# Performance work log

Hardware: AMD Instinct MI355X
Metric: run time of the kernel (lower is better)

Reference implementation:

```python
import jax, jax.numpy as jnp
import numpy as np

WBITS = 4   # weight bits (symmetric signed)
ABITS = 4   # activation bits (unsigned, [0,1])
CBITS = 4   # partial-sum quantization bits
ARRAY = 128 # crossbar array size (input-dim tile)
BN_EPS = 1e-5


def ste_round(x):
    # straight-through estimator round (identity gradient)
    return x + jax.lax.stop_gradient(jnp.round(x) - x)


def setup_inputs() -> dict:
    key = jax.random.key(0)
    k1, k2 = jax.random.split(key)
    B, FIN, FOUT = 65536, 256, 256
    x = jax.random.uniform(k1, (B, FIN), dtype=jnp.float32)        # quantized-act range [0,1]
    weight = jax.random.normal(k2, (FOUT, FIN), dtype=jnp.float32) * 0.05
    gamma = jnp.ones((FOUT,), jnp.float32)
    beta = jnp.zeros((FOUT,), jnp.float32)
    return {"x": x, "weight": weight, "gamma": gamma, "beta": beta}


def reference(x, weight, gamma, beta):
    qmax_w = 2 ** (WBITS - 1) - 1          # 7
    qmax_a = 2 ** ABITS - 1                # 15

    # --- symmetric weight quantization to WBITS (integer levels) ---
    scale_w = jnp.max(jnp.abs(weight)) / qmax_w
    w_int = ste_round(jnp.clip(weight / scale_w, -qmax_w, qmax_w))  # [Fout, Fin]

    # --- unsigned activation quantization to ABITS (integer levels) ---
    x_int = ste_round(jnp.clip(x, 0.0, 1.0) * qmax_a)               # [B, Fin]

    # --- crossbar-tiled integer matmul with partial-sum quantization ---
    B, Fin = x.shape
    Fout = weight.shape[0]
    T = Fin // ARRAY
    xt = x_int.reshape(B, T, ARRAY)          # [B, T, A]
    wt = w_int.reshape(Fout, T, ARRAY)       # [Fout, T, A]
    psum = jnp.einsum('bta,ota->bto', xt, wt)  # integer partial sums, [B, T, Fout]

    # quantize each partial sum to CBITS levels over the full tile dynamic range
    pmax = float(ARRAY * qmax_a * qmax_w)
    step = (2.0 * pmax) / (2 ** CBITS - 1)
    psum_q = ste_round(psum / step) * step

    acc = psum_q.sum(axis=1) * (scale_w / qmax_a)   # dequantized linear output [B, Fout]

    # --- BatchNorm1d (training mode: batch statistics) ---
    mu = acc.mean(axis=0)
    var = acc.var(axis=0)
    y = (acc - mu) * jax.lax.rsqrt(var + BN_EPS) * gamma + beta

    # --- quantized clipped-ReLU activation to ABITS ---
    out = ste_round(jnp.clip(y, 0.0, 1.0) * qmax_a) / qmax_a
    return out
```

## Files before the change

### kernel.cpp

```cpp
#include <hip/hip_runtime.h>
#include <cstdint>
#include <cstddef>

typedef int   v4i __attribute__((ext_vector_type(4)));
typedef float v4f __attribute__((ext_vector_type(4)));

static constexpr int NREP = 8;

static constexpr size_t WQ_OFF    = 0;
static constexpr size_t STATS_OFF = 65536;
static constexpr size_t PART_OFF  = STATS_OFF + NREP*512*4;
static constexpr size_t SBUF_OFF  = 131072 + 2048;
static constexpr size_t WS_NEEDED = SBUF_OFF + (size_t)65536 * 256;

__device__ __forceinline__ int rhe1792(int p) {
    unsigned u = (unsigned)(p + 17024);
    unsigned v = u >> 8;
    unsigned d = (v * 147u) >> 10;
    int q = (int)d - 9;
    unsigned tie = (unsigned)(((u & 255u) | (v - 7u * d)) == 0u);
    q -= (int)(tie & ((unsigned)q & 1u));
    return q;
}

__global__ void k_maxabs(const float* __restrict__ w, float* __restrict__ partials,
                         int* __restrict__ stats) {
    __shared__ float wmax[4];
    int idx = blockIdx.x * 256 + threadIdx.x;
    float4 f = ((const float4*)w)[idx];
    float m = fmaxf(fmaxf(fabsf(f.x), fabsf(f.y)), fmaxf(fabsf(f.z), fabsf(f.w)));
    #pragma unroll
    for (int s = 32; s > 0; s >>= 1) m = fmaxf(m, __shfl_xor(m, s, 64));
    if ((threadIdx.x & 63) == 0) wmax[threadIdx.x >> 6] = m;
    if (idx < NREP * 512) stats[idx] = 0;
    __syncthreads();
    if (threadIdx.x == 0)
        partials[blockIdx.x] = fmaxf(fmaxf(wmax[0], wmax[1]), fmaxf(wmax[2], wmax[3]));
}

__device__ __forceinline__ float reduce_partials(const float* __restrict__ partials, int tid) {
    float p = partials[tid & 63];
    #pragma unroll
    for (int s = 32; s > 0; s >>= 1) p = fmaxf(p, __shfl_xor(p, s, 64));
    return p;
}

__global__ void k_wquant(const float* __restrict__ w, const float* __restrict__ partials,
                         signed char* __restrict__ wq) {
    int idx = blockIdx.x * 256 + threadIdx.x;
    float scale = reduce_partials(partials, threadIdx.x) / 7.0f;
    float4 f = ((const float4*)w)[idx];
    int q0 = (int)rintf(fminf(fmaxf(f.x / scale, -7.f), 7.f));
    int q1 = (int)rintf(fminf(fmaxf(f.y / scale, -7.f), 7.f));
    int q2 = (int)rintf(fminf(fmaxf(f.z / scale, -7.f), 7.f));
    int q3 = (int)rintf(fminf(fmaxf(f.w / scale, -7.f), 7.f));
    ((int*)wq)[idx] = (q0 & 255) | ((q1 & 255) << 8) | ((q2 & 255) << 16) | ((q3 & 255) << 24);
}

template <typename ST>
__global__ __launch_bounds__(512, 4) void k_gemm(
    const float* __restrict__ x, const signed char* __restrict__ wq,
    ST* __restrict__ sbuf, int* __restrict__ stats)
{
    __shared__ __align__(16) signed char ldsx[64 * 272];
    const int tid  = threadIdx.x;
    const int lane = tid & 63;
    const int wv   = tid >> 6;
    const int obase = wv * 32;
    const int lr = lane & 15, quad = lane >> 4;
    const size_t rb0 = (size_t)blockIdx.x * 64;

    v4f f[8];
    const v4f* xb = (const v4f*)(x + rb0 * 256);
    #pragma unroll
    for (int j = 0; j < 8; ++j)
        f[j] = xb[j * 512 + tid];

    v4i wf[2][4];
    #pragma unroll
    for (int ot = 0; ot < 2; ++ot)
        #pragma unroll
        for (int kt = 0; kt < 4; ++kt)
            wf[ot][kt] = *(const v4i*)(wq + (size_t)(obase + ot * 16 + lr) * 256 + kt * 64 + quad * 16);

    #pragma unroll
    for (int j = 0; j < 8; ++j) {
        int idx = j * 512 + tid;
        int row = idx >> 6, c = idx & 63;
        int b0 = (int)rintf(fminf(fmaxf(f[j][0], 0.f), 1.f) * 15.f);
        int b1 = (int)rintf(fminf(fmaxf(f[j][1], 0.f), 1.f) * 15.f);
        int b2 = (int)rintf(fminf(fmaxf(f[j][2], 0.f), 1.f) * 15.f);
        int b3 = (int)rintf(fminf(fmaxf(f[j][3], 0.f), 1.f) * 15.f);
        *(int*)(ldsx + row * 272 + c * 4) = b0 | (b1 << 8) | (b2 << 16) | (b3 << 24);
    }
    __syncthreads();

    int ssum[2] = {0, 0};
    int ssq[2]  = {0, 0};

    #pragma unroll
    for (int t = 0; t < 4; ++t) {
        v4i a[4];
        #pragma unroll
        for (int kt = 0; kt < 4; ++kt)
            a[kt] = *(const v4i*)(ldsx + (t * 16 + lr) * 272 + kt * 64 + quad * 16);
        #pragma unroll
        for (int ot = 0; ot < 2; ++ot) {
            v4i acc0 = {0, 0, 0, 0}, acc1 = {0, 0, 0, 0};
            acc0 = __builtin_amdgcn_mfma_i32_16x16x64_i8(a[0], wf[ot][0], acc0, 0, 0, 0);
            acc0 = __builtin_amdgcn_mfma_i32_16x16x64_i8(a[1], wf[ot][1], acc0, 0, 0, 0);
            acc1 = __builtin_amdgcn_mfma_i32_16x16x64_i8(a[2], wf[ot][2], acc1, 0, 0, 0);
            acc1 = __builtin_amdgcn_mfma_i32_16x16x64_i8(a[3], wf[ot][3], acc1, 0, 0, 0);
            const int ocol = obase + ot * 16 + lr;
            if constexpr (sizeof(ST) == 1) {
                unsigned pack = 0;
                #pragma unroll
                for (int e = 0; e < 4; ++e) {
                    int s = rhe1792(acc0[e]) + rhe1792(acc1[e]);
                    ssum[ot] += s;
                    ssq[ot]  += s * s;
                    pack |= (unsigned)(s & 255) << (8 * e);
                }
                const size_t rg = (size_t)blockIdx.x * 16 + t * 4 + quad;
                ((unsigned*)sbuf)[rg * 256 + ocol] = pack;
            } else {
                ST* sp = sbuf + (rb0 + (size_t)t * 16 + quad * 4) * 256 + ocol;
                #pragma unroll
                for (int e = 0; e < 4; ++e) {
                    int s = rhe1792(acc0[e]) + rhe1792(acc1[e]);
                    ssum[ot] += s;
                    ssq[ot]  += s * s;
                    sp[(size_t)e * 256] = (ST)s;
                }
            }
        }
    }
    int* st = stats + (blockIdx.x & (NREP - 1)) * 512;
    #pragma unroll
    for (int ot = 0; ot < 2; ++ot) {
        int v = ssum[ot], u = ssq[ot];
        v += __shfl_xor(v, 16, 64); v += __shfl_xor(v, 32, 64);
        u += __shfl_xor(u, 16, 64); u += __shfl_xor(u, 32, 64);
        if (quad == 0) {
            atomicAdd(&st[obase + ot * 16 + lr], v);
            atomicAdd(&st[256 + obase + ot * 16 + lr], u);
        }
    }
}

template <typename LT>
__global__ __launch_bounds__(256) void k_out(const LT* sbuf, const int* __restrict__ stats,
                                             const float* __restrict__ partials,
                                             const float* __restrict__ gamma,
                                             const float* __restrict__ beta,
                                             float* out)
{
    __shared__ float2 ab[256];
    const int tid = threadIdx.x;
    {
        int o = tid;
        int s = 0, q = 0;
        #pragma unroll
        for (int rr = 0; rr < NREP; ++rr) {
            s += stats[rr * 512 + o];
            q += stats[rr * 512 + 256 + o];
        }
        float scale_w = reduce_partials(partials, o) / 7.0f;
        float t = scale_w / 15.0f;
        double Cs = 1792.0 * (double)t;
        const double N = 65536.0;
        double mean_s = (double)s / N;
        double var_s  = (double)q / N - mean_s * mean_s;
        double var    = Cs * Cs * var_s;
        double inv    = 1.0 / sqrt(var + 1e-5);
        double A = Cs * inv * (double)gamma[o];
        double B = (double)beta[o] - Cs * mean_s * inv * (double)gamma[o];
        ab[o] = make_float2((float)A, (float)B);
    }
    __syncthreads();

    const int b = blockIdx.x;
    const int d = ((b & 7) << 2) | ((b >> 3) & 3) | (b & ~31);
    const int ci = tid & 63;
    const int c0 = ci * 4;
    const float2 p0 = ab[c0], p1 = ab[c0 + 1], p2 = ab[c0 + 2], p3 = ab[c0 + 3];
    const float inv15 = 0.066666666666666666f;

    if constexpr (sizeof(LT) == 1) {
        const int rg = d * 4 + (tid >> 6);
        v4i V = ((const v4i*)sbuf)[(size_t)rg * 64 + ci];
        #pragma unroll
        for (int j = 0; j < 4; ++j) {
            float v0 = (float)((V[0] << (24 - 8 * j)) >> 24);
            float v1 = (float)((V[1] << (24 - 8 * j)) >> 24);
            float v2 = (float)((V[2] << (24 - 8 * j)) >> 24);
            float v3 = (float)((V[3] << (24 - 8 * j)) >> 24);
            float y0 = rintf(fminf(fmaxf(v0 * p0.x + p0.y, 0.f), 1.f) * 15.f);
            float y1 = rintf(fminf(fmaxf(v1 * p1.x + p1.y, 0.f), 1.f) * 15.f);
            float y2 = rintf(fminf(fmaxf(v2 * p2.x + p2.y, 0.f), 1.f) * 15.f);
            float y3 = rintf(fminf(fmaxf(v3 * p3.x + p3.y, 0.f), 1.f) * 15.f);
            v4f o = { y0 * inv15, y1 * inv15, y2 * inv15, y3 * inv15 };
            __builtin_nontemporal_store(o, (v4f*)out + (size_t)(4 * rg + j) * 64 + ci);
        }
    } else {
        const size_t base = (size_t)d * 1024 + tid;
        #pragma unroll
        for (int j = 0; j < 4; ++j) {
            const size_t F4 = base + (size_t)j * 256;
            v4f fl = ((const v4f*)sbuf)[F4];
            const int oo = (tid * 4) & 255;
            float2 q0 = ab[oo], q1 = ab[oo + 1], q2 = ab[oo + 2], q3 = ab[oo + 3];
            float y0 = rintf(fminf(fmaxf(fl[0] * q0.x + q0.y, 0.f), 1.f) * 15.f);
            float y1 = rintf(fminf(fmaxf(fl[1] * q1.x + q1.y, 0.f), 1.f) * 15.f);
            float y2 = rintf(fminf(fmaxf(fl[2] * q2.x + q2.y, 0.f), 1.f) * 15.f);
            float y3 = rintf(fminf(fmaxf(fl[3] * q3.x + q3.y, 0.f), 1.f) * 15.f);
            v4f o = { y0 * inv15, y1 * inv15, y2 * inv15, y3 * inv15 };
            __builtin_nontemporal_store(o, (v4f*)out + F4);
        }
    }
}

extern "C" void kernel_launch(void* const* d_in, const int* in_sizes, int n_in,
                              void* d_out, int out_size, void* d_ws, size_t ws_size,
                              hipStream_t stream)
{
    const float* x     = (const float*)d_in[0];
    const float* w     = (const float*)d_in[1];
    const float* gamma = (const float*)d_in[2];
    const float* beta  = (const float*)d_in[3];
    float* out = (float*)d_out;
    char* ws = (char*)d_ws;

    signed char* wq       = (signed char*)(ws + WQ_OFF);
    int*         stats    = (int*)(ws + STATS_OFF);
    float*       partials = (float*)(ws + PART_OFF);

    k_maxabs<<<dim3(64), dim3(256), 0, stream>>>(w, partials, stats);
    k_wquant<<<dim3(64), dim3(256), 0, stream>>>(w, partials, wq);

    if (ws_size >= WS_NEEDED) {
        signed char* sbuf = (signed char*)(ws + SBUF_OFF);
        k_gemm<signed char><<<dim3(1024), dim3(512), 0, stream>>>(x, wq, sbuf, stats);
        k_out<signed char><<<dim3(4096), dim3(256), 0, stream>>>(sbuf, stats, partials,
                                                                 gamma, beta, out);
    } else {
        k_gemm<float><<<dim3(1024), dim3(512), 0, stream>>>(x, wq, out, stats);
        k_out<float><<<dim3(4096), dim3(256), 0, stream>>>(out, stats, partials,
                                                           gamma, beta, out);
    }
}
```

Before: 132.3 us.

## Fuse GEMM and BatchNorm output into one cooperative kernel with grid sync

Adds a persistent cooperative kernel that quantizes x, runs the int8 MFMA crossbar GEMM with partial-sum quantization, and accumulates BN statistics. It then grid-syncs and applies BN plus the output quantization straight from register-held packed partial sums. This removes the int8 intermediate buffer's write and re-read through global memory and one kernel launch. Each block now handles 128 rows, so the grid is 512 blocks that must all be co-resident. The cost is a grid-wide barrier and a cooperative launch, with a fallback to the old path if the launch fails.

```diff
diff --git a/kernel.cpp b/kernel.cpp
--- a/kernel.cpp
+++ b/kernel.cpp
@@ -1,6 +1,9 @@
 #include <hip/hip_runtime.h>
+#include <hip/hip_cooperative_groups.h>
 #include <cstdint>
 #include <cstddef>
+
+namespace cg = cooperative_groups;
 
 typedef int   v4i __attribute__((ext_vector_type(4)));
 typedef float v4f __attribute__((ext_vector_type(4)));
@@ -11,7 +14,8 @@
 static constexpr size_t STATS_OFF = 65536;
 static constexpr size_t PART_OFF  = STATS_OFF + NREP*512*4;
 static constexpr size_t SBUF_OFF  = 131072 + 2048;
-static constexpr size_t WS_NEEDED = SBUF_OFF + (size_t)65536 * 256;
+static constexpr size_t WS_SBUF_NEEDED = SBUF_OFF + (size_t)65536 * 256;
+static constexpr size_t WS_MIN    = PART_OFF + 64 * 4;
 
 __device__ __forceinline__ int rhe1792(int p) {
     unsigned u = (unsigned)(p + 17024);
@@ -55,6 +59,154 @@
     int q2 = (int)rintf(fminf(fmaxf(f.z / scale, -7.f), 7.f));
     int q3 = (int)rintf(fminf(fmaxf(f.w / scale, -7.f), 7.f));
     ((int*)wq)[idx] = (q0 & 255) | ((q1 & 255) << 8) | ((q2 & 255) << 16) | ((q3 & 255) << 24);
+}
+
+__global__ __launch_bounds__(512, 4) void k_fused(
+    const float* __restrict__ x, const signed char* __restrict__ wq,
+    const float* __restrict__ partials, int* __restrict__ stats,
+    const float* __restrict__ gamma, const float* __restrict__ beta,
+    float* __restrict__ out)
+{
+    __shared__ __align__(16) signed char ldsx[128 * 272];
+    __shared__ __align__(16) float abA[256];
+    __shared__ __align__(16) float abB[256];
+
+    const int tid  = threadIdx.x;
+    const int lane = tid & 63;
+    const int wv   = tid >> 6;
+    const int obase = wv * 32;
+    const int lr = lane & 15, quad = lane >> 4;
+    const size_t rb0 = (size_t)blockIdx.x * 128;
+
+    v4f f[8];
+    const v4f* xb = (const v4f*)(x + rb0 * 256);
+    #pragma unroll
+    for (int j = 0; j < 8; ++j)
+        f[j] = xb[j * 512 + tid];
+
+    v4i wf[2][4];
+    #pragma unroll
+    for (int ot = 0; ot < 2; ++ot)
+        #pragma unroll
+        for (int kt = 0; kt < 4; ++kt)
+            wf[ot][kt] = *(const v4i*)(wq + (size_t)(obase + ot * 16 + lr) * 256 + kt * 64 + quad * 16);
+
+    #pragma unroll
+    for (int j = 0; j < 8; ++j) {
+        int idx = j * 512 + tid;
+        int row = idx >> 6, c = idx & 63;
+        int b0 = (int)rintf(fminf(fmaxf(f[j][0], 0.f), 1.f) * 15.f);
+        int b1 = (int)rintf(fminf(fmaxf(f[j][1], 0.f), 1.f) * 15.f);
+        int b2 = (int)rintf(fminf(fmaxf(f[j][2], 0.f), 1.f) * 15.f);
+        int b3 = (int)rintf(fminf(fmaxf(f[j][3], 0.f), 1.f) * 15.f);
+        *(int*)(ldsx + row * 272 + c * 4) = b0 | (b1 << 8) | (b2 << 16) | (b3 << 24);
+    }
+    #pragma unroll
+    for (int j = 0; j < 8; ++j)
+        f[j] = xb[4096 + j * 512 + tid];
+    #pragma unroll
+    for (int j = 0; j < 8; ++j) {
+        int idx = j * 512 + tid;
+        int row = 64 + (idx >> 6), c = idx & 63;
+        int b0 = (int)rintf(fminf(fmaxf(f[j][0], 0.f), 1.f) * 15.f);
+        int b1 = (int)rintf(fminf(fmaxf(f[j][1], 0.f), 1.f) * 15.f);
+        int b2 = (int)rintf(fminf(fmaxf(f[j][2], 0.f), 1.f) * 15.f);
+        int b3 = (int)rintf(fminf(fmaxf(f[j][3], 0.f), 1.f) * 15.f);
+        *(int*)(ldsx + row * 272 + c * 4) = b0 | (b1 << 8) | (b2 << 16) | (b3 << 24);
+    }
+    __syncthreads();
+
+    int ssum[2][4] = {{0,0,0,0},{0,0,0,0}};
+    int ssq [2][4] = {{0,0,0,0},{0,0,0,0}};
+    unsigned spack[16];
+
+    #pragma unroll
+    for (int t = 0; t < 8; ++t) {
+        v4i a[4];
+        #pragma unroll
+        for (int kt = 0; kt < 4; ++kt)
+            a[kt] = *(const v4i*)(ldsx + (t * 16 + lr) * 272 + kt * 64 + quad * 16);
+        #pragma unroll
+        for (int ot = 0; ot < 2; ++ot) {
+            v4i acc0 = {0, 0, 0, 0}, acc1 = {0, 0, 0, 0};
+            acc0 = __builtin_amdgcn_mfma_i32_16x16x64_i8(wf[ot][0], a[0], acc0, 0, 0, 0);
+            acc0 = __builtin_amdgcn_mfma_i32_16x16x64_i8(wf[ot][1], a[1], acc0, 0, 0, 0);
+            acc1 = __builtin_amdgcn_mfma_i32_16x16x64_i8(wf[ot][2], a[2], acc1, 0, 0, 0);
+            acc1 = __builtin_amdgcn_mfma_i32_16x16x64_i8(wf[ot][3], a[3], acc1, 0, 0, 0);
+            unsigned pack = 0;
+            #pragma unroll
+            for (int e = 0; e < 4; ++e) {
+                int s = rhe1792(acc0[e]) + rhe1792(acc1[e]);
+                ssum[ot][e] += s;
+                ssq [ot][e] += s * s;
+                pack |= (unsigned)(s & 255) << (8 * e);
+            }
+            spack[t * 2 + ot] = pack;
+        }
+    }
+
+    {
+        int* st = stats + (blockIdx.x & (NREP - 1)) * 512;
+        #pragma unroll
+        for (int ot = 0; ot < 2; ++ot)
+            #pragma unroll
+            for (int e = 0; e < 4; ++e) {
+                int v = ssum[ot][e], u = ssq[ot][e];
+                v += __shfl_xor(v, 1, 64); v += __shfl_xor(v, 2, 64);
+                v += __shfl_xor(v, 4, 64); v += __shfl_xor(v, 8, 64);
+                u += __shfl_xor(u, 1, 64); u += __shfl_xor(u, 2, 64);
+                u += __shfl_xor(u, 4, 64); u += __shfl_xor(u, 8, 64);
+                if (lr == 0) {
+                    int ch = obase + ot * 16 + quad * 4 + e;
+                    atomicAdd(&st[ch], v);
+                    atomicAdd(&st[256 + ch], u);
+                }
+            }
+    }
+
+    cg::this_grid().sync();
+
+    if (tid < 256) {
+        const int o = tid;
+        int s = 0, q = 0;
+        #pragma unroll
+        for (int rr = 0; rr < NREP; ++rr) {
+            s += __hip_atomic_load(&stats[rr * 512 + o],       __ATOMIC_RELAXED, __HIP_MEMORY_SCOPE_AGENT);
+            q += __hip_atomic_load(&stats[rr * 512 + 256 + o], __ATOMIC_RELAXED, __HIP_MEMORY_SCOPE_AGENT);
+        }
+        float scale_w = reduce_partials(partials, o) / 7.0f;
+        float t = scale_w / 15.0f;
+        double Cs = 1792.0 * (double)t;
+        const double N = 65536.0;
+        double mean_s = (double)s / N;
+        double var_s  = (double)q / N - mean_s * mean_s;
+        double var    = Cs * Cs * var_s;
+        double inv    = 1.0 / sqrt(var + 1e-5);
+        double A = Cs * inv * (double)gamma[o];
+        double B = (double)beta[o] - Cs * mean_s * inv * (double)gamma[o];
+        abA[o] = (float)A;
+        abB[o] = (float)B;
+    }
+    __syncthreads();
+
+    const float inv15 = 0.066666666666666666f;
+    #pragma unroll
+    for (int t = 0; t < 8; ++t)
+        #pragma unroll
+        for (int ot = 0; ot < 2; ++ot) {
+            unsigned pk = spack[t * 2 + ot];
+            const int ch0 = obase + ot * 16 + quad * 4;
+            v4f A4 = *(const v4f*)&abA[ch0];
+            v4f B4 = *(const v4f*)&abB[ch0];
+            v4f o4;
+            #pragma unroll
+            for (int e = 0; e < 4; ++e) {
+                float v = (float)((int)(pk << (24 - 8 * e)) >> 24);
+                o4[e] = rintf(fminf(fmaxf(v * A4[e] + B4[e], 0.f), 1.f) * 15.f) * inv15;
+            }
+            const size_t grow = rb0 + (size_t)t * 16 + lr;
+            __builtin_nontemporal_store(o4, (v4f*)out + grow * 64 + (ch0 >> 2));
+        }
 }
 
 template <typename ST>
@@ -238,14 +390,23 @@
     k_maxabs<<<dim3(64), dim3(256), 0, stream>>>(w, partials, stats);
     k_wquant<<<dim3(64), dim3(256), 0, stream>>>(w, partials, wq);
 
-    if (ws_size >= WS_NEEDED) {
-        signed char* sbuf = (signed char*)(ws + SBUF_OFF);
-        k_gemm<signed char><<<dim3(1024), dim3(512), 0, stream>>>(x, wq, sbuf, stats);
-        k_out<signed char><<<dim3(4096), dim3(256), 0, stream>>>(sbuf, stats, partials,
-                                                                 gamma, beta, out);
-    } else {
-        k_gemm<float><<<dim3(1024), dim3(512), 0, stream>>>(x, wq, out, stats);
-        k_out<float><<<dim3(4096), dim3(256), 0, stream>>>(out, stats, partials,
-                                                           gamma, beta, out);
-    }
-}
+    hipError_t err = hipErrorUnknown;
+    if (ws_size >= WS_MIN) {
+        void* kargs[] = { (void*)&x, (void*)&wq, (void*)&partials, (void*)&stats,
+                          (void*)&gamma, (void*)&beta, (void*)&out };
+        err = hipLaunchCooperativeKernel((const void*)k_fused, dim3(512), dim3(512),
+                                         kargs, 0, stream);
+    }
+    if (err != hipSuccess) {
+        if (ws_size >= WS_SBUF_NEEDED) {
+            signed char* sbuf = (signed char*)(ws + SBUF_OFF);
+            k_gemm<signed char><<<dim3(1024), dim3(512), 0, stream>>>(x, wq, sbuf, stats);
+            k_out<signed char><<<dim3(4096), dim3(256), 0, stream>>>(sbuf, stats, partials,
+                                                                     gamma, beta, out);
+        } else {
+            k_gemm<float><<<dim3(1024), dim3(512), 0, stream>>>(x, wq, out, stats);
+            k_out<float><<<dim3(4096), dim3(256), 0, stream>>>(out, stats, partials,
+                                                               gamma, beta, out);
+        }
+    }
+}
```

New measurement: 238.4 us. 1.8x slower.
